# Optimization experiments

Measured on AMD Instinct MI355X. Metric: run time of the kernel, lower is better.

## Reference

```python
import jax, jax.numpy as jnp
import numpy as np

CUTOFF = 1.5  # matches init cutoff
BIG = 1e6    # stand-in for masked-out (diagonal) distances


def _energy(positions, cell, sigma_matrix, epsilon_matrix, alpha_matrix, species):
    n = positions.shape[0]
    # pairwise displacements dr[i, j] = pos[j] - pos[i], minimum image under PBC
    dr = positions[None, :, :] - positions[:, None, :]          # [N, N, 3]
    inv_cell = jnp.linalg.inv(cell)
    frac = dr @ inv_cell
    frac = frac - jnp.round(frac)                               # minimum image
    dr = frac @ cell
    r2 = jnp.sum(dr * dr, axis=-1)                              # [N, N]
    eye = jnp.eye(n, dtype=bool)
    r = jnp.sqrt(jnp.where(eye, 1.0, r2))                       # safe sqrt on diag
    r = jnp.where(eye, BIG, r)                                  # mask self-pairs
    # species-pair parameter gather: [N, N]
    si, sj = species[:, None], species[None, :]
    sig = sigma_matrix[si, sj]
    eps = epsilon_matrix[si, sj]
    alp = alpha_matrix[si, sj]
    within = (r < CUTOFF) & (~eye)
    # soft-sphere pair energy: eps/alpha * (1 - r/sigma)^alpha for r < sigma
    f = jnp.maximum(1.0 - r / sig, 0.0)
    e = (eps / alp) * jnp.power(f, alp)
    e = jnp.where(within, e, 0.0)
    return jnp.sum(e) / 2.0


def setup_inputs() -> dict:
    key = jax.random.key(0)
    k1, k2, k3, k4, k5 = jax.random.split(key, 5)
    N, S = 4096, 8
    density = 0.8
    L = float((N / density) ** (1.0 / 3.0))
    positions = jax.random.uniform(k1, (N, 3), dtype=jnp.float32) * L
    cell = (L * jnp.eye(3)).astype(jnp.float32)
    species = jax.random.randint(k2, (N,), 0, S)

    def sym(k, base, scale):
        a = jax.random.uniform(k, (S, S), dtype=jnp.float32)
        a = 0.5 * (a + a.T)
        return base + scale * a

    sigma_matrix = sym(k3, 0.9, 0.2)    # ~1.0
    epsilon_matrix = sym(k4, 0.9, 0.2)  # ~1.0
    alpha_matrix = sym(k5, 2.0, 0.5)    # ~2.0-2.5
    return {
        "positions": positions,
        "cell": cell,
        "sigma_matrix": sigma_matrix,
        "epsilon_matrix": epsilon_matrix,
        "alpha_matrix": alpha_matrix,
        "species": species,
    }


def reference(positions, cell, sigma_matrix, epsilon_matrix, alpha_matrix, species):
    energy, g = jax.value_and_grad(
        lambda p: _energy(p, cell, sigma_matrix, epsilon_matrix, alpha_matrix, species)
    )(positions)
    forces = -g
    return energy, forces
```

## Files before the change

kernel.cpp:

```cpp
#include <hip/hip_runtime.h>


#define TI 256
#define TJ 64
#define CUT2 2.25f

__device__ __forceinline__ float fast_pow(float f, float e) {
    return __builtin_amdgcn_exp2f(e * __builtin_amdgcn_logf(f));
}

__global__ __launch_bounds__(TI) void soft_sphere_kernel(
    const float* __restrict__ pos,
    const float* __restrict__ cell,
    const float* __restrict__ sigm,
    const float* __restrict__ epsm,
    const float* __restrict__ alpm,
    const int*   __restrict__ spec,
    float* __restrict__ out,
    int n)
{
    __shared__ float4 sh_pos[TJ];
    __shared__ float4 sh_tab[64];
    __shared__ float  sh_e[TI / 64];

    const int tid = threadIdx.x;
    const int j0  = blockIdx.y * TJ;

    if (tid < 64) {
        float sg = sigm[tid], ep = epsm[tid], al = alpm[tid];
        float inv_sg = 1.0f / sg;
        sh_tab[tid] = make_float4(inv_sg, al - 1.0f, ep / al, ep * inv_sg);
        int j = j0 + tid;
        sh_pos[tid] = make_float4(pos[3 * j + 0], pos[3 * j + 1],
                                  pos[3 * j + 2], __int_as_float(spec[j]));
    }

    const float m00 = cell[0], m01 = cell[1], m02 = cell[2];
    const float m10 = cell[3], m11 = cell[4], m12 = cell[5];
    const float m20 = cell[6], m21 = cell[7], m22 = cell[8];
    const bool diag = (m01 == 0.0f) & (m02 == 0.0f) & (m10 == 0.0f) &
                      (m12 == 0.0f) & (m20 == 0.0f) & (m21 == 0.0f);

    const int   i   = blockIdx.x * TI + tid;
    const float px  = pos[3 * i + 0];
    const float py  = pos[3 * i + 1];
    const float pz  = pos[3 * i + 2];
    const int   si8 = spec[i] << 3;

    __syncthreads();

    float e_acc = 0.0f, fxa = 0.0f, fya = 0.0f, fza = 0.0f;

    if (diag) {
        const float iLx = 1.0f / m00, iLy = 1.0f / m11, iLz = 1.0f / m22;
#pragma unroll 4
        for (int t = 0; t < TJ; ++t) {
            float4 pj = sh_pos[t];
            float dx = pj.x - px;
            float dy = pj.y - py;
            float dz = pj.z - pz;
            dx = fmaf(-rintf(dx * iLx), m00, dx);
            dy = fmaf(-rintf(dy * iLy), m11, dy);
            dz = fmaf(-rintf(dz * iLz), m22, dz);
            float r2 = fmaf(dx, dx, fmaf(dy, dy, dz * dz));
            if (r2 < CUT2 && (j0 + t) != i) {
                float4 tab = sh_tab[si8 + __float_as_int(pj.w)];
                float rinv = rsqrtf(r2);
                float r    = r2 * rinv;
                float f    = fmaf(-r, tab.x, 1.0f);
                if (f > 0.0f) {
                    float p = fast_pow(f, tab.y);
                    e_acc = fmaf(tab.z * p, f, e_acc);
                    float c = tab.w * p * rinv;
                    fxa = fmaf(-c, dx, fxa);
                    fya = fmaf(-c, dy, fya);
                    fza = fmaf(-c, dz, fza);
                }
            }
        }
    } else {
        const float det = m00 * (m11 * m22 - m12 * m21)
                        - m01 * (m10 * m22 - m12 * m20)
                        + m02 * (m10 * m21 - m11 * m20);
        const float rdet = 1.0f / det;
        const float i00 = (m11 * m22 - m12 * m21) * rdet;
        const float i01 = (m02 * m21 - m01 * m22) * rdet;
        const float i02 = (m01 * m12 - m02 * m11) * rdet;
        const float i10 = (m12 * m20 - m10 * m22) * rdet;
        const float i11 = (m00 * m22 - m02 * m20) * rdet;
        const float i12 = (m02 * m10 - m00 * m12) * rdet;
        const float i20 = (m10 * m21 - m11 * m20) * rdet;
        const float i21 = (m01 * m20 - m00 * m21) * rdet;
        const float i22 = (m00 * m11 - m01 * m10) * rdet;
#pragma unroll 2
        for (int t = 0; t < TJ; ++t) {
            float4 pj = sh_pos[t];
            float dx = pj.x - px, dy = pj.y - py, dz = pj.z - pz;
            float fx = dx * i00 + dy * i10 + dz * i20;
            float fy = dx * i01 + dy * i11 + dz * i21;
            float fz = dx * i02 + dy * i12 + dz * i22;
            fx -= rintf(fx); fy -= rintf(fy); fz -= rintf(fz);
            float ddx = fx * m00 + fy * m10 + fz * m20;
            float ddy = fx * m01 + fy * m11 + fz * m21;
            float ddz = fx * m02 + fy * m12 + fz * m22;
            float r2 = fmaf(ddx, ddx, fmaf(ddy, ddy, ddz * ddz));
            if (r2 < CUT2 && (j0 + t) != i) {
                float4 tab = sh_tab[si8 + __float_as_int(pj.w)];
                float rinv = rsqrtf(r2);
                float r    = r2 * rinv;
                float f    = fmaf(-r, tab.x, 1.0f);
                if (f > 0.0f) {
                    float p = fast_pow(f, tab.y);
                    e_acc = fmaf(tab.z * p, f, e_acc);
                    float c = tab.w * p * rinv;
                    fxa = fmaf(-c, ddx, fxa);
                    fya = fmaf(-c, ddy, fya);
                    fza = fmaf(-c, ddz, fza);
                }
            }
        }
    }

    atomicAdd(&out[1 + 3 * i + 0], fxa);
    atomicAdd(&out[1 + 3 * i + 1], fya);
    atomicAdd(&out[1 + 3 * i + 2], fza);

    for (int off = 32; off > 0; off >>= 1)
        e_acc += __shfl_down(e_acc, off, 64);
    if ((tid & 63) == 0) sh_e[tid >> 6] = e_acc;
    __syncthreads();
    if (tid == 0) {
        float tot = 0.0f;
        for (int w = 0; w < TI / 64; ++w) tot += sh_e[w];
        atomicAdd(&out[0], 0.5f * tot);
    }
}

extern "C" void kernel_launch(void* const* d_in, const int* in_sizes, int n_in,
                              void* d_out, int out_size, void* d_ws, size_t ws_size,
                              hipStream_t stream) {
    const float* pos  = (const float*)d_in[0];
    const float* cell = (const float*)d_in[1];
    const float* sigm = (const float*)d_in[2];
    const float* epsm = (const float*)d_in[3];
    const float* alpm = (const float*)d_in[4];
    const int*   spec = (const int*)d_in[5];
    float* out = (float*)d_out;
    const int n = in_sizes[5];

    (void)hipMemsetAsync(out, 0, (size_t)out_size * sizeof(float), stream);

    dim3 grid(n / TI, (n + TJ - 1) / TJ);
    soft_sphere_kernel<<<grid, TI, 0, stream>>>(pos, cell, sigm, epsm, alpm,
                                                spec, out, n);
}
```

Baseline: 92.72 us.

## Replace force atomics with workspace partials and a separate reduction kernel

Per-block force and energy partials now go to a workspace array, and a second kernel sums them deterministically. This removes the global atomics and the memset. The pair loop also computes a cheaper min-image distance with fabs/fmin and does the rint-based wrap only for pairs inside the cutoff. The cutoff is tightened to the largest sigma squared from the species table. The cost is an extra kernel launch and about 3 MB of workspace traffic. NCHUNK is hardcoded to 64, so the layout only matches n=4096.

New measurement: 94.93 us. 1.02x slower.

```diff
diff --git a/kernel.cpp b/kernel.cpp
--- a/kernel.cpp
+++ b/kernel.cpp
@@ -3,25 +3,27 @@
 
 #define TI 256
 #define TJ 64
+#define NCHUNK 64
 #define CUT2 2.25f
 
 __device__ __forceinline__ float fast_pow(float f, float e) {
     return __builtin_amdgcn_exp2f(e * __builtin_amdgcn_logf(f));
 }
 
-__global__ __launch_bounds__(TI) void soft_sphere_kernel(
+__global__ __launch_bounds__(TI) void pair_kernel(
     const float* __restrict__ pos,
     const float* __restrict__ cell,
     const float* __restrict__ sigm,
     const float* __restrict__ epsm,
     const float* __restrict__ alpm,
     const int*   __restrict__ spec,
-    float* __restrict__ out,
+    float* __restrict__ ws,
     int n)
 {
     __shared__ float4 sh_pos[TJ];
     __shared__ float4 sh_tab[64];
-    __shared__ float  sh_e[TI / 64];
+    __shared__ float  sh_red[TI / 64];
+    __shared__ float  sh_thr2;
 
     const int tid = threadIdx.x;
     const int j0  = blockIdx.y * TJ;
@@ -33,6 +35,10 @@
         int j = j0 + tid;
         sh_pos[tid] = make_float4(pos[3 * j + 0], pos[3 * j + 1],
                                   pos[3 * j + 2], __int_as_float(spec[j]));
+        float mx = sg * sg;
+        for (int off = 32; off > 0; off >>= 1)
+            mx = fmaxf(mx, __shfl_down(mx, off, 64));
+        if (tid == 0) sh_thr2 = fminf(mx, CUT2);
     }
 
     const float m00 = cell[0], m01 = cell[1], m02 = cell[2];
@@ -48,22 +54,28 @@
     const int   si8 = spec[i] << 3;
 
     __syncthreads();
+    const float thr2 = sh_thr2;
 
     float e_acc = 0.0f, fxa = 0.0f, fya = 0.0f, fza = 0.0f;
 
     if (diag) {
-        const float iLx = 1.0f / m00, iLy = 1.0f / m11, iLz = 1.0f / m22;
+        const float Lx = m00, Ly = m11, Lz = m22;
+        const float iLx = 1.0f / Lx, iLy = 1.0f / Ly, iLz = 1.0f / Lz;
 #pragma unroll 4
         for (int t = 0; t < TJ; ++t) {
             float4 pj = sh_pos[t];
             float dx = pj.x - px;
             float dy = pj.y - py;
             float dz = pj.z - pz;
-            dx = fmaf(-rintf(dx * iLx), m00, dx);
-            dy = fmaf(-rintf(dy * iLy), m11, dy);
-            dz = fmaf(-rintf(dz * iLz), m22, dz);
-            float r2 = fmaf(dx, dx, fmaf(dy, dy, dz * dz));
-            if (r2 < CUT2 && (j0 + t) != i) {
+            float ax = fabsf(dx), ay = fabsf(dy), az = fabsf(dz);
+            float wx = fminf(ax, Lx - ax);
+            float wy = fminf(ay, Ly - ay);
+            float wz = fminf(az, Lz - az);
+            float r2 = fmaf(wx, wx, fmaf(wy, wy, wz * wz));
+            if (r2 < thr2 && (j0 + t) != i) {
+                float sx = fmaf(-rintf(dx * iLx), Lx, dx);
+                float sy = fmaf(-rintf(dy * iLy), Ly, dy);
+                float sz = fmaf(-rintf(dz * iLz), Lz, dz);
                 float4 tab = sh_tab[si8 + __float_as_int(pj.w)];
                 float rinv = rsqrtf(r2);
                 float r    = r2 * rinv;
@@ -72,9 +84,9 @@
                     float p = fast_pow(f, tab.y);
                     e_acc = fmaf(tab.z * p, f, e_acc);
                     float c = tab.w * p * rinv;
-                    fxa = fmaf(-c, dx, fxa);
-                    fya = fmaf(-c, dy, fya);
-                    fza = fmaf(-c, dz, fza);
+                    fxa = fmaf(-c, sx, fxa);
+                    fya = fmaf(-c, sy, fya);
+                    fza = fmaf(-c, sz, fza);
                 }
             }
         }
@@ -104,7 +116,7 @@
             float ddy = fx * m01 + fy * m11 + fz * m21;
             float ddz = fx * m02 + fy * m12 + fz * m22;
             float r2 = fmaf(ddx, ddx, fmaf(ddy, ddy, ddz * ddz));
-            if (r2 < CUT2 && (j0 + t) != i) {
+            if (r2 < thr2 && (j0 + t) != i) {
                 float4 tab = sh_tab[si8 + __float_as_int(pj.w)];
                 float rinv = rsqrtf(r2);
                 float r    = r2 * rinv;
@@ -121,18 +133,46 @@
         }
     }
 
-    atomicAdd(&out[1 + 3 * i + 0], fxa);
-    atomicAdd(&out[1 + 3 * i + 1], fya);
-    atomicAdd(&out[1 + 3 * i + 2], fza);
+    const int axs  = n * NCHUNK;
+    const int base = blockIdx.y * n + i;
+    ws[0 * axs + base] = fxa;
+    ws[1 * axs + base] = fya;
+    ws[2 * axs + base] = fza;
 
     for (int off = 32; off > 0; off >>= 1)
         e_acc += __shfl_down(e_acc, off, 64);
-    if ((tid & 63) == 0) sh_e[tid >> 6] = e_acc;
+    if ((tid & 63) == 0) sh_red[tid >> 6] = e_acc;
     __syncthreads();
     if (tid == 0) {
         float tot = 0.0f;
-        for (int w = 0; w < TI / 64; ++w) tot += sh_e[w];
-        atomicAdd(&out[0], 0.5f * tot);
+        for (int w = 0; w < TI / 64; ++w) tot += sh_red[w];
+        ws[3 * axs + blockIdx.y * gridDim.x + blockIdx.x] = tot;
+    }
+}
+
+__global__ __launch_bounds__(256) void reduce_kernel(
+    const float* __restrict__ ws,
+    float* __restrict__ out,
+    int n, int nblk_e)
+{
+    const int gtid = blockIdx.x * 256 + threadIdx.x;
+    const int axis = gtid / n;
+    const int i    = gtid - axis * n;
+    const int axs  = n * NCHUNK;
+
+    const float* p = ws + axis * axs + i;
+    float s = 0.0f;
+#pragma unroll
+    for (int c = 0; c < NCHUNK; ++c) s += p[c * n];
+    out[1 + 3 * i + axis] = s;
+
+    if (blockIdx.x == 0 && threadIdx.x < 64) {
+        const float* e = ws + 3 * axs;
+        float es = 0.0f;
+        for (int k = threadIdx.x; k < nblk_e; k += 64) es += e[k];
+        for (int off = 32; off > 0; off >>= 1)
+            es += __shfl_down(es, off, 64);
+        if (threadIdx.x == 0) out[0] = 0.5f * es;
     }
 }
 
@@ -146,11 +186,12 @@
     const float* alpm = (const float*)d_in[4];
     const int*   spec = (const int*)d_in[5];
     float* out = (float*)d_out;
+    float* ws  = (float*)d_ws;
     const int n = in_sizes[5];
 
-    (void)hipMemsetAsync(out, 0, (size_t)out_size * sizeof(float), stream);
-
-    dim3 grid(n / TI, (n + TJ - 1) / TJ);
-    soft_sphere_kernel<<<grid, TI, 0, stream>>>(pos, cell, sigm, epsm, alpm,
-                                                spec, out, n);
+    dim3 gridA(n / TI, NCHUNK);
+    pair_kernel<<<gridA, TI, 0, stream>>>(pos, cell, sigm, epsm, alpm,
+                                          spec, ws, n);
+    reduce_kernel<<<(3 * n) / 256, 256, 0, stream>>>(ws, out, n,
+                                                     gridA.x * gridA.y);
 }
```
